# Optimization experiments

Hardware: AMD Instinct MI355X
Metric: run time of the kernel (lower is better)

The kernel has to match this reference:

```python
import jax, jax.numpy as jnp
import numpy as np

B = 8192
INPUT_DIM = 1024
HIDDEN = 4096
LATENT = 256
K = 16384  # codebook size
COMMIT = 0.25


def setup_inputs() -> dict:
    key = jax.random.key(0)
    ks = jax.random.split(key, 12)

    def lin(k, fan_in, fan_out):
        bound = 1.0 / np.sqrt(fan_in)
        kw, kb = jax.random.split(k)
        W = jax.random.uniform(kw, (fan_in, fan_out), jnp.float32, -bound, bound)
        b = jax.random.uniform(kb, (fan_out,), jnp.float32, -bound, bound)
        return W, b

    eW1, eb1 = lin(ks[0], INPUT_DIM, HIDDEN)
    eW2, eb2 = lin(ks[1], HIDDEN, HIDDEN)
    eW3, eb3 = lin(ks[2], HIDDEN, LATENT)
    dW1, db1 = lin(ks[3], LATENT, HIDDEN)
    dW2, db2 = lin(ks[4], HIDDEN, HIDDEN)
    dW3, db3 = lin(ks[5], HIDDEN, INPUT_DIM)
    codebook = jax.random.uniform(ks[6], (K, LATENT), jnp.float32, -1.0 / K, 1.0 / K)
    x = jax.random.normal(ks[7], (B, INPUT_DIM), jnp.float32)
    return {
        "x": x,
        "eW1": eW1, "eb1": eb1, "eW2": eW2, "eb2": eb2, "eW3": eW3, "eb3": eb3,
        "codebook": codebook,
        "dW1": dW1, "db1": db1, "dW2": dW2, "db2": db2, "dW3": dW3, "db3": db3,
    }


def _encoder(x, eW1, eb1, eW2, eb2, eW3, eb3):
    h = jax.nn.relu(x @ eW1 + eb1)          # dropout is identity in eval
    h = jax.nn.relu(h @ eW2 + eb2)
    return jnp.tanh(h @ eW3 + eb3)          # [B, LATENT]


def _decoder(z, dW1, db1, dW2, db2, dW3, db3):
    h = jax.nn.relu(z @ dW1 + db1)
    h = jax.nn.relu(h @ dW2 + db2)
    return h @ dW3 + db3                    # [B, INPUT_DIM]


def _vq(z, codebook):
    # pairwise squared distances: ||z||^2 + ||e||^2 - 2 z.e^T   -> [B, K]
    d = (jnp.sum(z * z, axis=1, keepdims=True)
         + jnp.sum(codebook * codebook, axis=1)
         - 2.0 * (z @ codebook.T))
    idx = jnp.argmin(d, axis=1)                              # [B]
    enc = jax.nn.one_hot(idx, K, dtype=jnp.float32)          # [B, K]
    q = enc @ codebook                                       # [B, LATENT]
    e_loss = jnp.mean((jax.lax.stop_gradient(q) - z) ** 2)
    q_loss = jnp.mean((q - jax.lax.stop_gradient(z)) ** 2)
    vq_loss = q_loss + COMMIT * e_loss
    q_st = z + jax.lax.stop_gradient(q - z)                  # straight-through
    avg_probs = jnp.mean(enc, axis=0)
    perplexity = jnp.exp(-jnp.sum(avg_probs * jnp.log(avg_probs + 1e-10)))
    return q_st, idx, vq_loss, perplexity


def reference(x, eW1, eb1, eW2, eb2, eW3, eb3, codebook,
              dW1, db1, dW2, db2, dW3, db3):
    z = _encoder(x, eW1, eb1, eW2, eb2, eW3, eb3)
    q, tokens, vq_loss, perplexity = _vq(z, codebook)
    recon = _decoder(q, dW1, db1, dW2, db2, dW3, db3)
    recon_loss = jnp.mean((recon - x) ** 2)
    total = vq_loss + recon_loss
    return recon, tokens, vq_loss, recon_loss, total, perplexity
```

## Files before the change

kernel.cpp:

```cpp
#include <hip/hip_runtime.h>
#include <stdint.h>

#define B_N 8192
#define D_IN 1024
#define D_HID 4096
#define D_LAT 256
#define K_CB 16384
#define VQ_NB (K_CB / 128)

typedef __attribute__((ext_vector_type(8))) short bf16x8;
typedef __attribute__((ext_vector_type(4))) float f32x4;

__device__ __forceinline__ unsigned short f2b(float v) {
  unsigned u = __float_as_uint(v);
  u += 0x7fffu + ((u >> 16) & 1u);
  return (unsigned short)(u >> 16);
}

#define XCD_SWIZZLE(bx, by)                                   \
  {                                                           \
    const int gx_ = gridDim.x, n_ = gx_ * gridDim.y;          \
    const int wg_ = (by)*gx_ + (bx);                          \
    const int q_ = n_ >> 3;                                   \
    const int s_ = (wg_ & 7) * q_ + (wg_ >> 3);               \
    (bx) = s_ % gx_;                                          \
    (by) = s_ / gx_;                                          \
  }

__device__ __forceinline__ void enc_big_body(
    const float* __restrict__ A, const float* __restrict__ Bm,
    const float* __restrict__ bias, float* __restrict__ C, int M, int N,
    int K) {
  __shared__ float As[16 * 260];
  __shared__ float Bs[16 * 128];
  const int tid = threadIdx.x;
  const int w = tid >> 6;
  const int tx = tid & 15, ty = tid >> 4;
  int bx = blockIdx.x, by = blockIdx.y;
  XCD_SWIZZLE(bx, by)
  const int m0 = by << 8, n0 = bx << 7;

  float acc[16][8];
#pragma unroll
  for (int i = 0; i < 16; ++i)
#pragma unroll
    for (int j = 0; j < 8; ++j) acc[i][j] = 0.0f;

  for (int k0 = 0; k0 < K; k0 += 16) {
#pragma unroll
    for (int r = 0; r < 4; ++r) {
      const int f = tid + (r << 8);
      const int m = f >> 2, kq = (f & 3) << 2;
      const float4 v = *(const float4*)(A + (size_t)(m0 + m) * K + k0 + kq);
      As[(kq + 0) * 260 + m] = v.x;
      As[(kq + 1) * 260 + m] = v.y;
      As[(kq + 2) * 260 + m] = v.z;
      As[(kq + 3) * 260 + m] = v.w;
    }
#pragma unroll
    for (int r = 0; r < 2; ++r) {
      const int f = tid + (r << 8);
      const float* gp = Bm + (size_t)(k0 + (f >> 5)) * N + n0 + ((f & 31) << 2);
      __builtin_amdgcn_global_load_lds((const unsigned int*)gp,
                                       (unsigned int*)&Bs[(r << 10) + (w << 8)],
                                       16, 0, 0);
    }
    __syncthreads();
#pragma unroll
    for (int kk = 0; kk < 16; ++kk) {
      float a[16], b[8];
#pragma unroll
      for (int q = 0; q < 4; ++q)
        *(float4*)(a + (q << 2)) =
            *(const float4*)(&As[kk * 260 + (q << 6) + (ty << 2)]);
      *(float4*)(b) = *(const float4*)(&Bs[kk * 128 + (tx << 2)]);
      *(float4*)(b + 4) = *(const float4*)(&Bs[kk * 128 + 64 + (tx << 2)]);
#pragma unroll
      for (int i = 0; i < 16; ++i)
#pragma unroll
        for (int j = 0; j < 8; ++j) acc[i][j] = fmaf(a[i], b[j], acc[i][j]);
    }
    __syncthreads();
  }

  float bb[8];
  *(float4*)(bb) = *(const float4*)(bias + n0 + (tx << 2));
  *(float4*)(bb + 4) = *(const float4*)(bias + n0 + 64 + (tx << 2));
#pragma unroll
  for (int i = 0; i < 16; ++i) {
    const int row = m0 + ((i >> 2) << 6) + (ty << 2) + (i & 3);
    float vrow[8];
#pragma unroll
    for (int j = 0; j < 8; ++j) vrow[j] = fmaxf(acc[i][j] + bb[j], 0.0f);
    *(float4*)(C + (size_t)row * N + n0 + (tx << 2)) = *(float4*)(vrow);
    *(float4*)(C + (size_t)row * N + n0 + 64 + (tx << 2)) = *(float4*)(vrow + 4);
  }
}

__global__ __launch_bounds__(256, 2) void enc1_k(const float* A, const float* B,
                                                 const float* bias, float* C,
                                                 int M, int N, int K) {
  enc_big_body(A, B, bias, C, M, N, K);
}
__global__ __launch_bounds__(256, 2) void enc2_k(const float* A, const float* B,
                                                 const float* bias, float* C,
                                                 int M, int N, int K) {
  enc_big_body(A, B, bias, C, M, N, K);
}

__global__ __launch_bounds__(256, 2) void enc_small_k(
    const float* __restrict__ A, const float* __restrict__ Bm,
    const float* __restrict__ bias, float* __restrict__ C, int M, int N,
    int K) {
  __shared__ float As[16][128];
  __shared__ float Bs[16][128];
  const int tid = threadIdx.x;
  const int tx = tid & 15, ty = tid >> 4;
  const int m0 = blockIdx.y << 7, n0 = blockIdx.x << 7;
  float acc[8][8];
#pragma unroll
  for (int i = 0; i < 8; ++i)
#pragma unroll
    for (int j = 0; j < 8; ++j) acc[i][j] = 0.0f;
  for (int k0 = 0; k0 < K; k0 += 16) {
#pragma unroll
    for (int r = 0; r < 2; ++r) {
      const int f = tid + (r << 8);
      const int m = f >> 2, kq = (f & 3) << 2;
      const float4 v = *(const float4*)(A + (size_t)(m0 + m) * K + k0 + kq);
      As[kq + 0][m] = v.x; As[kq + 1][m] = v.y;
      As[kq + 2][m] = v.z; As[kq + 3][m] = v.w;
    }
#pragma unroll
    for (int r = 0; r < 2; ++r) {
      const int f = tid + (r << 8);
      const int k = f >> 5, nq = (f & 31) << 2;
      *(float4*)(&Bs[k][nq]) =
          *(const float4*)(Bm + (size_t)(k0 + k) * N + n0 + nq);
    }
    __syncthreads();
#pragma unroll
    for (int kk = 0; kk < 16; ++kk) {
      float a[8], b[8];
      *(float4*)(a) = *(const float4*)(&As[kk][ty << 2]);
      *(float4*)(a + 4) = *(const float4*)(&As[kk][64 + (ty << 2)]);
      *(float4*)(b) = *(const float4*)(&Bs[kk][tx << 2]);
      *(float4*)(b + 4) = *(const float4*)(&Bs[kk][64 + (tx << 2)]);
#pragma unroll
      for (int i = 0; i < 8; ++i)
#pragma unroll
        for (int j = 0; j < 8; ++j) acc[i][j] = fmaf(a[i], b[j], acc[i][j]);
    }
    __syncthreads();
  }
  float bb[8];
  *(float4*)(bb) = *(const float4*)(bias + n0 + (tx << 2));
  *(float4*)(bb + 4) = *(const float4*)(bias + n0 + 64 + (tx << 2));
#pragma unroll
  for (int i = 0; i < 8; ++i) {
    const int row = m0 + ((i < 4) ? (ty << 2) + i : 64 + (ty << 2) + i - 4);
    float vrow[8];
#pragma unroll
    for (int j = 0; j < 8; ++j) vrow[j] = fmaxf(acc[i][j] + bb[j], 0.0f);
    *(float4*)(C + (size_t)row * N + n0 + (tx << 2)) = *(float4*)(vrow);
    *(float4*)(C + (size_t)row * N + n0 + 64 + (tx << 2)) = *(float4*)(vrow + 4);
  }
}

__global__ __launch_bounds__(256, 2) void enc3_part_k(
    const float* __restrict__ A, const float* __restrict__ B,
    float* __restrict__ P, int M, int K) {
  __shared__ float As[16][128];
  __shared__ float Bs[16][128];
  const int tid = threadIdx.x;
  const int tx = tid & 15, ty = tid >> 4;
  const int m0 = blockIdx.y << 7, n0 = blockIdx.x << 7;
  const int s = blockIdx.z;
  const int kbeg = s * (K >> 3), kend = kbeg + (K >> 3);
  float acc[8][8];
#pragma unroll
  for (int i = 0; i < 8; ++i)
#pragma unroll
    for (int j = 0; j < 8; ++j) acc[i][j] = 0.0f;
  for (int k0 = kbeg; k0 < kend; k0 += 16) {
#pragma unroll
    for (int r = 0; r < 2; ++r) {
      const int f = tid + (r << 8);
      const int m = f >> 2, kq = (f & 3) << 2;
      const float4 v = *(const float4*)(A + (size_t)(m0 + m) * K + k0 + kq);
      As[kq + 0][m] = v.x; As[kq + 1][m] = v.y;
      As[kq + 2][m] = v.z; As[kq + 3][m] = v.w;
    }
#pragma unroll
    for (int r = 0; r < 2; ++r) {
      const int f = tid + (r << 8);
      const int k = f >> 5, nq = (f & 31) << 2;
      *(float4*)(&Bs[k][nq]) =
          *(const float4*)(B + (size_t)(k0 + k) * D_LAT + n0 + nq);
    }
    __syncthreads();
#pragma unroll
    for (int kk = 0; kk < 16; ++kk) {
      float a[8], b[8];
      *(float4*)(a) = *(const float4*)(&As[kk][ty << 2]);
      *(float4*)(a + 4) = *(const float4*)(&As[kk][64 + (ty << 2)]);
      *(float4*)(b) = *(const float4*)(&Bs[kk][tx << 2]);
      *(float4*)(b + 4) = *(const float4*)(&Bs[kk][64 + (tx << 2)]);
#pragma unroll
      for (int i = 0; i < 8; ++i)
#pragma unroll
        for (int j = 0; j < 8; ++j) acc[i][j] = fmaf(a[i], b[j], acc[i][j]);
    }
    __syncthreads();
  }
  float* Ps = P + (size_t)s * M * D_LAT;
#pragma unroll
  for (int i = 0; i < 8; ++i) {
    const int row = m0 + ((i < 4) ? (ty << 2) + i : 64 + (ty << 2) + i - 4);
    *(float4*)(Ps + (size_t)row * D_LAT + n0 + (tx << 2)) = *(float4*)(&acc[i][0]);
    *(float4*)(Ps + (size_t)row * D_LAT + n0 + 64 + (tx << 2)) = *(float4*)(&acc[i][4]);
  }
}

__global__ void enc3_comb_k(const float* __restrict__ P,
                            const float* __restrict__ bias,
                            float* __restrict__ z, int M) {
  const size_t i4 = (size_t)blockIdx.x * blockDim.x + threadIdx.x;
  const size_t tot = (size_t)M * (D_LAT / 4);
  if (i4 >= tot) return;
  const size_t sstr = (size_t)M * (D_LAT / 4);
  const float4* Pv = (const float4*)P;
  float sx = 0.f, sy = 0.f, sz = 0.f, sw = 0.f;
#pragma unroll
  for (int s = 0; s < 8; ++s) {
    const float4 v = Pv[i4 + (size_t)s * sstr];
    sx += v.x; sy += v.y; sz += v.z; sw += v.w;
  }
  const int col = (int)((i4 << 2) & (D_LAT - 1));
  const float4 bb = *(const float4*)(bias + col);
  float4 o;
  o.x = tanhf(sx + bb.x);
  o.y = tanhf(sy + bb.y);
  o.z = tanhf(sz + bb.z);
  o.w = tanhf(sw + bb.w);
  ((float4*)z)[i4] = o;
}

__global__ __launch_bounds__(256, 2) void vq_k256(
    const float* __restrict__ A, const float* __restrict__ Bm,
    const float* __restrict__ zz, const float* __restrict__ ee,
    unsigned long long* __restrict__ keys2) {
  __shared__ float As[16 * 260];
  __shared__ float Bs[16 * 132];
  const int tid = threadIdx.x;
  const int tx = tid & 15, ty = tid >> 4;
  int bx = blockIdx.x, by = blockIdx.y;
  XCD_SWIZZLE(bx, by)
  const int m0 = by << 8, n0 = bx << 7;
  const int K = D_LAT;

  float acc[16][8];
#pragma unroll
  for (int i = 0; i < 16; ++i)
#pragma unroll
    for (int j = 0; j < 8; ++j) acc[i][j] = 0.0f;

  for (int k0 = 0; k0 < K; k0 += 16) {
#pragma unroll
    for (int r = 0; r < 4; ++r) {
      const int f = tid + (r << 8);
      const int m = f >> 2, kq = (f & 3) << 2;
      const float4 v = *(const float4*)(A + (size_t)(m0 + m) * K + k0 + kq);
      As[(kq + 0) * 260 + m] = v.x;
      As[(kq + 1) * 260 + m] = v.y;
      As[(kq + 2) * 260 + m] = v.z;
      As[(kq + 3) * 260 + m] = v.w;
    }
#pragma unroll
    for (int r = 0; r < 2; ++r) {
      const int f = tid + (r << 8);
      const int n = f >> 2, kq = (f & 3) << 2;
      const float4 v = *(const float4*)(Bm + (size_t)(n0 + n) * K + k0 + kq);
      Bs[(kq + 0) * 132 + n] = v.x;
      Bs[(kq + 1) * 132 + n] = v.y;
      Bs[(kq + 2) * 132 + n] = v.z;
      Bs[(kq + 3) * 132 + n] = v.w;
    }
    __syncthreads();
#pragma unroll
    for (int kk = 0; kk < 16; ++kk) {
      float a[16], b[8];
#pragma unroll
      for (int q = 0; q < 4; ++q)
        *(float4*)(a + (q << 2)) =
            *(const float4*)(&As[kk * 260 + (q << 6) + (ty << 2)]);
      *(float4*)(b) = *(const float4*)(&Bs[kk * 132 + (tx << 2)]);
      *(float4*)(b + 4) = *(const float4*)(&Bs[kk * 132 + 64 + (tx << 2)]);
#pragma unroll
      for (int i = 0; i < 16; ++i)
#pragma unroll
        for (int j = 0; j < 8; ++j) acc[i][j] = fmaf(a[i], b[j], acc[i][j]);
    }
    __syncthreads();
  }

  float zr[16];
#pragma unroll
  for (int i = 0; i < 16; ++i)
    zr[i] = zz[m0 + ((i >> 2) << 6) + (ty << 2) + (i & 3)];
  float ev[8];
  *(float4*)(ev) = *(const float4*)(ee + n0 + (tx << 2));
  *(float4*)(ev + 4) = *(const float4*)(ee + n0 + 64 + (tx << 2));
#pragma unroll
  for (int i = 0; i < 16; ++i) {
    unsigned long long bk = ~0ull;
#pragma unroll
    for (int j = 0; j < 8; ++j) {
      const int col = n0 + ((j >> 2) << 6) + (tx << 2) + (j & 3);
      const float t = zr[i] + ev[j];
      const float d = t - 2.0f * acc[i][j];
      unsigned u = __float_as_uint(d);
      u = (u & 0x80000000u) ? ~u : (u | 0x80000000u);
      const unsigned long long key = ((unsigned long long)u << 32) | (unsigned)col;
      bk = key < bk ? key : bk;
    }
#pragma unroll
    for (int s = 1; s <= 8; s <<= 1) {
      const unsigned long long o = __shfl_xor(bk, s);
      if (o < bk) bk = o;
    }
    if (tx == 0) {
      const int row = m0 + ((i >> 2) << 6) + (ty << 2) + (i & 3);
      keys2[(size_t)row * VQ_NB + bx] = bk;
    }
  }
}

__global__ void vq_red_k(const unsigned long long* __restrict__ keys2,
                         unsigned long long* __restrict__ keys) {
  const int row = (int)((blockIdx.x * blockDim.x + threadIdx.x) >> 6);
  const int lane = threadIdx.x & 63;
  if (row >= B_N) return;
  unsigned long long a = keys2[(size_t)row * VQ_NB + lane];
  const unsigned long long b = keys2[(size_t)row * VQ_NB + 64 + lane];
  a = b < a ? b : a;
#pragma unroll
  for (int s = 32; s; s >>= 1) {
    const unsigned long long o = __shfl_xor(a, s);
    a = o < a ? o : a;
  }
  if (lane == 0) keys[row] = a;
}

template <int EPI>
__device__ __forceinline__ void mgemm_body(
    const unsigned short* __restrict__ A, const unsigned short* __restrict__ Bt,
    const float* __restrict__ bias, void* __restrict__ Cout, int M, int N,
    int K, const float* __restrict__ xref, double* __restrict__ accums) {
  __shared__ __align__(16) unsigned short As[4096];
  __shared__ __align__(16) unsigned short Bs[4096];
  const int tid = threadIdx.x;
  const int w = tid >> 6, l = tid & 63;
  const int wr = w >> 1, wc = w & 1;
  const int g = l >> 4, tx = l & 15;
  int bx = blockIdx.x, by = blockIdx.y;
  XCD_SWIZZLE(bx, by)
  const int m0 = by << 7, n0 = bx << 7;

  f32x4 acc[4][4];
#pragma unroll
  for (int i = 0; i < 4; ++i)
#pragma unroll
    for (int j = 0; j < 4; ++j) acc[i][j] = (f32x4)0.0f;

  for (int k0 = 0; k0 < K; k0 += 32) {
#pragma unroll
    for (int c = 0; c < 2; ++c) {
      const int f = tid + (c << 8);
      const unsigned short* ga =
          A + (size_t)(m0 + (f >> 2)) * K + k0 + ((f & 3) << 3);
      __builtin_amdgcn_global_load_lds((const unsigned int*)ga,
                                       (unsigned int*)&As[(c << 11) + (w << 9)],
                                       16, 0, 0);
      const unsigned short* gb =
          Bt + (size_t)(n0 + (f >> 2)) * K + k0 + ((f & 3) << 3);
      __builtin_amdgcn_global_load_lds((const unsigned int*)gb,
                                       (unsigned int*)&Bs[(c << 11) + (w << 9)],
                                       16, 0, 0);
    }
    __syncthreads();
    bf16x8 af[4], bfv[4];
#pragma unroll
    for (int f = 0; f < 4; ++f) {
      af[f] = *(const bf16x8*)&As[((wr << 6) + (f << 4) + tx) * 32 + (g << 3)];
      bfv[f] = *(const bf16x8*)&Bs[((wc << 6) + (f << 4) + tx) * 32 + (g << 3)];
    }
#pragma unroll
    for (int fm = 0; fm < 4; ++fm)
#pragma unroll
      for (int fn = 0; fn < 4; ++fn)
        acc[fm][fn] = __builtin_amdgcn_mfma_f32_16x16x32_bf16(
            af[fm], bfv[fn], acc[fm][fn], 0, 0, 0);
    __syncthreads();
  }

  double lsum = 0.0;
#pragma unroll
  for (int fm = 0; fm < 4; ++fm) {
    const int row0 = m0 + (wr << 6) + (fm << 4) + (g << 2);
#pragma unroll
    for (int fn = 0; fn < 4; ++fn) {
      const int col = n0 + (wc << 6) + (fn << 4) + tx;
      const float bb = bias[col];
#pragma unroll
      for (int r = 0; r < 4; ++r) {
        float v = acc[fm][fn][r] + bb;
        if (EPI == 0) {
          v = fmaxf(v, 0.0f);
          ((unsigned short*)Cout)[(size_t)(row0 + r) * N + col] = f2b(v);
        } else {
          const float xr = xref[(size_t)(row0 + r) * N + col];
          const float df = v - xr;
          lsum += (double)df * (double)df;
          ((float*)Cout)[(size_t)(row0 + r) * N + col] = v;
        }
      }
    }
  }
  if (EPI == 1) {
#pragma unroll
    for (int o = 32; o; o >>= 1) lsum += __shfl_down(lsum, o);
    if (l == 0) atomicAdd(accums + 1, lsum);
  }
}

__global__ __launch_bounds__(256, 2) void dec1_k(const unsigned short* A,
                                                 const unsigned short* Bt,
                                                 const float* bias,
                                                 unsigned short* C, int M,
                                                 int N, int K) {
  mgemm_body<0>(A, Bt, bias, C, M, N, K, nullptr, nullptr);
}
__global__ __launch_bounds__(256, 2) void dec2_k(const unsigned short* A,
                                                 const unsigned short* Bt,
                                                 const float* bias,
                                                 unsigned short* C, int M,
                                                 int N, int K) {
  mgemm_body<0>(A, Bt, bias, C, M, N, K, nullptr, nullptr);
}
__global__ __launch_bounds__(256, 2) void dec3_k(const unsigned short* A,
                                                 const unsigned short* Bt,
                                                 const float* bias, float* C,
                                                 int M, int N, int K,
                                                 const float* xref,
                                                 double* accums) {
  mgemm_body<1>(A, Bt, bias, C, M, N, K, xref, accums);
}

__global__ void castT_k(const float* __restrict__ W,
                        unsigned short* __restrict__ out, int K, int N) {
  __shared__ float t[32][33];
  const int tx = threadIdx.x & 31, ty4 = threadIdx.x >> 5;
  const int nb = blockIdx.x << 5, kb = blockIdx.y << 5;
#pragma unroll
  for (int r = 0; r < 4; ++r) {
    const int k = (ty4 << 2) + r;
    t[k][tx] = W[(size_t)(kb + k) * N + nb + tx];
  }
  __syncthreads();
#pragma unroll
  for (int r = 0; r < 4; ++r) {
    const int n = (ty4 << 2) + r;
    out[(size_t)(nb + n) * K + kb + tx] = f2b(t[tx][n]);
  }
}

__global__ void rowsumsq(const float* __restrict__ v, float* __restrict__ out,
                         int rows) {
  const int w = (int)((blockIdx.x * blockDim.x + threadIdx.x) >> 6);
  const int lane = threadIdx.x & 63;
  if (w >= rows) return;
  const float4 x = *(const float4*)(v + (size_t)w * 256 + (lane << 2));
  float s = ((x.x * x.x + x.y * x.y) + x.z * x.z) + x.w * x.w;
#pragma unroll
  for (int o = 32; o; o >>= 1) s += __shfl_down(s, o);
  if (lane == 0) out[w] = s;
}

__global__ void finalize_vq(const unsigned long long* __restrict__ keys,
                            const float* __restrict__ z,
                            const float* __restrict__ cb,
                            unsigned short* __restrict__ qst_bf,
                            float* __restrict__ tok, int* __restrict__ counts,
                            double* __restrict__ accums) {
  const int row = (int)((blockIdx.x * blockDim.x + threadIdx.x) >> 6);
  const int lane = threadIdx.x & 63;
  if (row >= B_N) return;
  const int idx = (int)(keys[row] & 0xffffffffull);
  const float4 zv = *(const float4*)(z + (size_t)row * 256 + (lane << 2));
  const float4 evv = *(const float4*)(cb + (size_t)idx * 256 + (lane << 2));
  float4 q;
  double s = 0.0;
  float d;
  d = evv.x - zv.x; q.x = zv.x + d; s += (double)d * (double)d;
  d = evv.y - zv.y; q.y = zv.y + d; s += (double)d * (double)d;
  d = evv.z - zv.z; q.z = zv.z + d; s += (double)d * (double)d;
  d = evv.w - zv.w; q.w = zv.w + d; s += (double)d * (double)d;
  ushort4 qb;
  qb.x = f2b(q.x); qb.y = f2b(q.y); qb.z = f2b(q.z); qb.w = f2b(q.w);
  *(ushort4*)(qst_bf + (size_t)row * 256 + (lane << 2)) = qb;
#pragma unroll
  for (int o = 32; o; o >>= 1) s += __shfl_down(s, o);
  if (lane == 0) {
    atomicAdd(accums + 0, s);
    tok[row] = (float)idx;
    atomicAdd(counts + idx, 1);
  }
}

__global__ void finalize_scalars(const int* __restrict__ counts,
                                 const double* __restrict__ accums,
                                 float* __restrict__ outs) {
  __shared__ double red[256];
  double h = 0.0;
  for (int k = threadIdx.x; k < K_CB; k += 256) {
    const float p = (float)counts[k] * (1.0f / 8192.0f);
    const float t = p * logf(p + 1e-10f);
    h += (double)t;
  }
  red[threadIdx.x] = h;
  __syncthreads();
  for (int s = 128; s; s >>= 1) {
    if ((int)threadIdx.x < s) red[threadIdx.x] += red[threadIdx.x + s];
    __syncthreads();
  }
  if (threadIdx.x == 0) {
    const float perp = expf((float)(-red[0]));
    const float m1 = (float)(accums[0] * (1.0 / ((double)B_N * (double)D_LAT)));
    const float vq = m1 + 0.25f * m1;
    const float rl = (float)(accums[1] * (1.0 / ((double)B_N * (double)D_IN)));
    outs[0] = vq;
    outs[1] = rl;
    outs[2] = vq + rl;
    outs[3] = perp;
  }
}

extern "C" void kernel_launch(void* const* d_in, const int* in_sizes, int n_in,
                              void* d_out, int out_size, void* d_ws,
                              size_t ws_size, hipStream_t stream) {
  (void)in_sizes; (void)n_in; (void)out_size;
  const float* x   = (const float*)d_in[0];
  const float* eW1 = (const float*)d_in[1];
  const float* eb1 = (const float*)d_in[2];
  const float* eW2 = (const float*)d_in[3];
  const float* eb2 = (const float*)d_in[4];
  const float* eW3 = (const float*)d_in[5];
  const float* eb3 = (const float*)d_in[6];
  const float* cb  = (const float*)d_in[7];
  const float* dW1 = (const float*)d_in[8];
  const float* db1 = (const float*)d_in[9];
  const float* dW2 = (const float*)d_in[10];
  const float* db2 = (const float*)d_in[11];
  const float* dW3 = (const float*)d_in[12];
  const float* db3 = (const float*)d_in[13];
  float* out = (float*)d_out;

  char* ws = (char*)d_ws;
  const size_t OFF_Z      = 0;
  const size_t OFF_EEV    = OFF_Z + (size_t)B_N * D_LAT * 4;
  const size_t OFF_ZZV    = OFF_EEV + (size_t)K_CB * 4;
  const size_t OFF_KEYS   = OFF_ZZV + (size_t)B_N * 4;
  const size_t OFF_COUNTS = OFF_KEYS + (size_t)B_N * 8;
  const size_t OFF_ACC    = OFF_COUNTS + (size_t)K_CB * 4;
  const size_t OFF_QB     = OFF_ACC + 256;
  const size_t OFF_K2     = OFF_QB + (size_t)B_N * D_LAT * 2;
  const size_t OFF_H      = OFF_K2 + (size_t)B_N * VQ_NB * 8;

  float* z    = (float*)(ws + OFF_Z);
  float* eev  = (float*)(ws + OFF_EEV);
  float* zzv  = (float*)(ws + OFF_ZZV);
  unsigned long long* keys = (unsigned long long*)(ws + OFF_KEYS);
  int* counts = (int*)(ws + OFF_COUNTS);
  double* accums = (double*)(ws + OFF_ACC);
  unsigned short* qst_bf = (unsigned short*)(ws + OFF_QB);
  unsigned long long* keys2 = (unsigned long long*)(ws + OFF_K2);

  int c_enc = 256;
  for (int c = 8192; c >= 256; c >>= 1)
    if (OFF_H + 2ull * c * D_HID * 4 <= ws_size) { c_enc = c; break; }
  float* hA = (float*)(ws + OFF_H);
  float* hB = hA + (size_t)c_enc * D_HID;
  float* P3 = hA;

  const size_t SZ_WB1 = (size_t)D_HID * D_LAT * 2;
  const size_t SZ_WB2 = (size_t)D_HID * D_HID * 2;
  const size_t SZ_WB3 = (size_t)D_IN * D_HID * 2;
  const size_t OFF_DECH = OFF_H + SZ_WB1 + SZ_WB2 + SZ_WB3;
  int c_dec = 128;
  for (int c = 8192; c >= 128; c >>= 1)
    if (OFF_DECH + 2ull * c * D_HID * 2 <= ws_size) { c_dec = c; break; }
  unsigned short* wB1 = (unsigned short*)(ws + OFF_H);
  unsigned short* wB2 = (unsigned short*)(ws + OFF_H + SZ_WB1);
  unsigned short* wB3 = (unsigned short*)(ws + OFF_H + SZ_WB1 + SZ_WB2);
  unsigned short* hbfA = (unsigned short*)(ws + OFF_DECH);
  unsigned short* hbfB = hbfA + (size_t)c_dec * D_HID;

  float* tok_out = out + (size_t)B_N * D_IN;
  float* scal_out = tok_out + B_N;

  hipMemsetAsync(counts, 0, (size_t)K_CB * 4, stream);
  hipMemsetAsync(accums, 0, 2 * sizeof(double), stream);

  rowsumsq<<<(K_CB * 64) / 256, 256, 0, stream>>>(cb, eev, K_CB);

  const bool big = (c_enc >= 4096);
  for (int c0 = 0; c0 < B_N; c0 += c_enc) {
    if (big) {
      enc1_k<<<dim3(D_HID / 128, c_enc / 256), 256, 0, stream>>>(
          x + (size_t)c0 * D_IN, eW1, eb1, hA, c_enc, D_HID, D_IN);
      enc2_k<<<dim3(D_HID / 128, c_enc / 256), 256, 0, stream>>>(
          hA, eW2, eb2, hB, c_enc, D_HID, D_HID);
    } else {
      const dim3 gH(D_HID / 128, c_enc / 128);
      enc_small_k<<<gH, 256, 0, stream>>>(x + (size_t)c0 * D_IN, eW1, eb1, hA,
                                          c_enc, D_HID, D_IN);
      enc_small_k<<<gH, 256, 0, stream>>>(hA, eW2, eb2, hB, c_enc, D_HID,
                                          D_HID);
    }
    enc3_part_k<<<dim3(D_LAT / 128, c_enc / 128, 8), 256, 0, stream>>>(
        hB, eW3, P3, c_enc, D_HID);
    enc3_comb_k<<<(c_enc * (D_LAT / 4) + 255) / 256, 256, 0, stream>>>(
        P3, eb3, z + (size_t)c0 * D_LAT, c_enc);
  }

  rowsumsq<<<(B_N * 64) / 256, 256, 0, stream>>>(z, zzv, B_N);

  vq_k256<<<dim3(VQ_NB, B_N / 256), 256, 0, stream>>>(z, cb, zzv, eev, keys2);
  vq_red_k<<<(B_N * 64) / 256, 256, 0, stream>>>(keys2, keys);
  finalize_vq<<<(B_N * 64) / 256, 256, 0, stream>>>(keys, z, cb, qst_bf,
                                                    tok_out, counts, accums);

  castT_k<<<dim3(D_HID / 32, D_LAT / 32), 256, 0, stream>>>(dW1, wB1, D_LAT, D_HID);
  castT_k<<<dim3(D_HID / 32, D_HID / 32), 256, 0, stream>>>(dW2, wB2, D_HID, D_HID);
  castT_k<<<dim3(D_IN / 32, D_HID / 32), 256, 0, stream>>>(dW3, wB3, D_HID, D_IN);

  for (int c0 = 0; c0 < B_N; c0 += c_dec) {
    const dim3 gH(D_HID / 128, c_dec / 128);
    dec1_k<<<gH, 256, 0, stream>>>(qst_bf + (size_t)c0 * D_LAT, wB1, db1, hbfA,
                                   c_dec, D_HID, D_LAT);
    dec2_k<<<gH, 256, 0, stream>>>(hbfA, wB2, db2, hbfB, c_dec, D_HID, D_HID);
    dec3_k<<<dim3(D_IN / 128, c_dec / 128), 256, 0, stream>>>(
        hbfB, wB3, db3, out + (size_t)c0 * D_IN, c_dec, D_IN, D_HID,
        x + (size_t)c0 * D_IN, accums);
  }

  finalize_scalars<<<1, 256, 0, stream>>>(counts, accums, scal_out);
}
```

Measured before the change: 5.649 ms.

## Keep encoder activations transposed and load A tiles via global_load_lds

```diff
diff --git a/kernel.cpp b/kernel.cpp
--- a/kernel.cpp
+++ b/kernel.cpp
@@ -27,11 +27,29 @@
     (by) = s_ / gx_;                                          \
   }
 
-__device__ __forceinline__ void enc_big_body(
-    const float* __restrict__ A, const float* __restrict__ Bm,
-    const float* __restrict__ bias, float* __restrict__ C, int M, int N,
+__global__ void transF_k(const float* __restrict__ in, float* __restrict__ out,
+                         int R, int C) {
+  __shared__ float t[32][33];
+  const int tx = threadIdx.x & 31, ty4 = threadIdx.x >> 5;
+  const int rb = blockIdx.y << 5, cb_ = blockIdx.x << 5;
+#pragma unroll
+  for (int r = 0; r < 4; ++r) {
+    const int lr = (ty4 << 2) + r;
+    t[lr][tx] = in[(size_t)(rb + lr) * C + cb_ + tx];
+  }
+  __syncthreads();
+#pragma unroll
+  for (int r = 0; r < 4; ++r) {
+    const int lr = (ty4 << 2) + r;
+    out[(size_t)(cb_ + lr) * R + rb + tx] = t[tx][lr];
+  }
+}
+
+__device__ __forceinline__ void enc_bigT_body(
+    const float* __restrict__ AT_, const float* __restrict__ Bm,
+    const float* __restrict__ bias, float* __restrict__ CT, int M, int N,
     int K) {
-  __shared__ float As[16 * 260];
+  __shared__ float As[16 * 256];
   __shared__ float Bs[16 * 128];
   const int tid = threadIdx.x;
   const int w = tid >> 6;
@@ -50,12 +68,10 @@
 #pragma unroll
     for (int r = 0; r < 4; ++r) {
       const int f = tid + (r << 8);
-      const int m = f >> 2, kq = (f & 3) << 2;
-      const float4 v = *(const float4*)(A + (size_t)(m0 + m) * K + k0 + kq);
-      As[(kq + 0) * 260 + m] = v.x;
-      As[(kq + 1) * 260 + m] = v.y;
-      As[(kq + 2) * 260 + m] = v.z;
-      As[(kq + 3) * 260 + m] = v.w;
+      const float* gp = AT_ + (size_t)(k0 + (f >> 6)) * M + m0 + ((f & 63) << 2);
+      __builtin_amdgcn_global_load_lds((const unsigned int*)gp,
+                                       (unsigned int*)&As[(r << 10) + (w << 8)],
+                                       16, 0, 0);
     }
 #pragma unroll
     for (int r = 0; r < 2; ++r) {
@@ -72,7 +88,7 @@
 #pragma unroll
       for (int q = 0; q < 4; ++q)
         *(float4*)(a + (q << 2)) =
-            *(const float4*)(&As[kk * 260 + (q << 6) + (ty << 2)]);
+            *(const float4*)(&As[kk * 256 + (q << 6) + (ty << 2)]);
       *(float4*)(b) = *(const float4*)(&Bs[kk * 128 + (tx << 2)]);
       *(float4*)(b + 4) = *(const float4*)(&Bs[kk * 128 + 64 + (tx << 2)]);
 #pragma unroll
@@ -87,25 +103,31 @@
   *(float4*)(bb) = *(const float4*)(bias + n0 + (tx << 2));
   *(float4*)(bb + 4) = *(const float4*)(bias + n0 + 64 + (tx << 2));
 #pragma unroll
-  for (int i = 0; i < 16; ++i) {
-    const int row = m0 + ((i >> 2) << 6) + (ty << 2) + (i & 3);
-    float vrow[8];
-#pragma unroll
-    for (int j = 0; j < 8; ++j) vrow[j] = fmaxf(acc[i][j] + bb[j], 0.0f);
-    *(float4*)(C + (size_t)row * N + n0 + (tx << 2)) = *(float4*)(vrow);
-    *(float4*)(C + (size_t)row * N + n0 + 64 + (tx << 2)) = *(float4*)(vrow + 4);
-  }
-}
-
-__global__ __launch_bounds__(256, 2) void enc1_k(const float* A, const float* B,
-                                                 const float* bias, float* C,
+  for (int j = 0; j < 8; ++j) {
+    const int col = n0 + ((j >> 2) << 6) + (tx << 2) + (j & 3);
+#pragma unroll
+    for (int q = 0; q < 4; ++q) {
+      float vq4[4];
+#pragma unroll
+      for (int r = 0; r < 4; ++r)
+        vq4[r] = fmaxf(acc[(q << 2) + r][j] + bb[j], 0.0f);
+      *(float4*)(CT + (size_t)col * M + m0 + (q << 6) + (ty << 2)) =
+          *(float4*)(vq4);
+    }
+  }
+}
+
+__global__ __launch_bounds__(256, 2) void enc1_k(const float* AT_,
+                                                 const float* B,
+                                                 const float* bias, float* CT,
                                                  int M, int N, int K) {
-  enc_big_body(A, B, bias, C, M, N, K);
-}
-__global__ __launch_bounds__(256, 2) void enc2_k(const float* A, const float* B,
-                                                 const float* bias, float* C,
+  enc_bigT_body(AT_, B, bias, CT, M, N, K);
+}
+__global__ __launch_bounds__(256, 2) void enc2_k(const float* AT_,
+                                                 const float* B,
+                                                 const float* bias, float* CT,
                                                  int M, int N, int K) {
-  enc_big_body(A, B, bias, C, M, N, K);
+  enc_bigT_body(AT_, B, bias, CT, M, N, K);
 }
 
 __global__ __launch_bounds__(256, 2) void enc_small_k(
@@ -167,12 +189,14 @@
   }
 }
 
+template <bool AT>
 __global__ __launch_bounds__(256, 2) void enc3_part_k(
     const float* __restrict__ A, const float* __restrict__ B,
-    float* __restrict__ P, int M, int K) {
-  __shared__ float As[16][128];
-  __shared__ float Bs[16][128];
+    float* __restrict__ P, int M, int K, int Mstr) {
+  __shared__ float As[16 * 128];
+  __shared__ float Bs[16 * 128];
   const int tid = threadIdx.x;
+  const int w = tid >> 6;
   const int tx = tid & 15, ty = tid >> 4;
   const int m0 = blockIdx.y << 7, n0 = blockIdx.x << 7;
   const int s = blockIdx.z;
@@ -183,29 +207,42 @@
 #pragma unroll
     for (int j = 0; j < 8; ++j) acc[i][j] = 0.0f;
   for (int k0 = kbeg; k0 < kend; k0 += 16) {
+    if (AT) {
+#pragma unroll
+      for (int r = 0; r < 2; ++r) {
+        const int f = tid + (r << 8);
+        const float* gp =
+            A + (size_t)(k0 + (f >> 5)) * Mstr + m0 + ((f & 31) << 2);
+        __builtin_amdgcn_global_load_lds(
+            (const unsigned int*)gp, (unsigned int*)&As[(r << 10) + (w << 8)],
+            16, 0, 0);
+      }
+    } else {
+#pragma unroll
+      for (int r = 0; r < 2; ++r) {
+        const int f = tid + (r << 8);
+        const int m = f >> 2, kq = (f & 3) << 2;
+        const float4 v = *(const float4*)(A + (size_t)(m0 + m) * K + k0 + kq);
+        As[(kq + 0) * 128 + m] = v.x; As[(kq + 1) * 128 + m] = v.y;
+        As[(kq + 2) * 128 + m] = v.z; As[(kq + 3) * 128 + m] = v.w;
+      }
+    }
 #pragma unroll
     for (int r = 0; r < 2; ++r) {
       const int f = tid + (r << 8);
-      const int m = f >> 2, kq = (f & 3) << 2;
-      const float4 v = *(const float4*)(A + (size_t)(m0 + m) * K + k0 + kq);
-      As[kq + 0][m] = v.x; As[kq + 1][m] = v.y;
-      As[kq + 2][m] = v.z; As[kq + 3][m] = v.w;
-    }
-#pragma unroll
-    for (int r = 0; r < 2; ++r) {
-      const int f = tid + (r << 8);
-      const int k = f >> 5, nq = (f & 31) << 2;
-      *(float4*)(&Bs[k][nq]) =
-          *(const float4*)(B + (size_t)(k0 + k) * D_LAT + n0 + nq);
+      const float* gp = B + (size_t)(k0 + (f >> 5)) * D_LAT + n0 + ((f & 31) << 2);
+      __builtin_amdgcn_global_load_lds((const unsigned int*)gp,
+                                       (unsigned int*)&Bs[(r << 10) + (w << 8)],
+                                       16, 0, 0);
     }
     __syncthreads();
 #pragma unroll
     for (int kk = 0; kk < 16; ++kk) {
       float a[8], b[8];
-      *(float4*)(a) = *(const float4*)(&As[kk][ty << 2]);
-      *(float4*)(a + 4) = *(const float4*)(&As[kk][64 + (ty << 2)]);
-      *(float4*)(b) = *(const float4*)(&Bs[kk][tx << 2]);
-      *(float4*)(b + 4) = *(const float4*)(&Bs[kk][64 + (tx << 2)]);
+      *(float4*)(a) = *(const float4*)(&As[kk * 128 + (ty << 2)]);
+      *(float4*)(a + 4) = *(const float4*)(&As[kk * 128 + 64 + (ty << 2)]);
+      *(float4*)(b) = *(const float4*)(&Bs[kk * 128 + (tx << 2)]);
+      *(float4*)(b + 4) = *(const float4*)(&Bs[kk * 128 + 64 + (tx << 2)]);
 #pragma unroll
       for (int i = 0; i < 8; ++i)
 #pragma unroll
@@ -247,17 +284,17 @@
 }
 
 __global__ __launch_bounds__(256, 2) void vq_k256(
-    const float* __restrict__ A, const float* __restrict__ Bm,
+    const float* __restrict__ zT, const float* __restrict__ cbT,
     const float* __restrict__ zz, const float* __restrict__ ee,
     unsigned long long* __restrict__ keys2) {
-  __shared__ float As[16 * 260];
-  __shared__ float Bs[16 * 132];
+  __shared__ float As[16 * 256];
+  __shared__ float Bs[16 * 128];
   const int tid = threadIdx.x;
+  const int w = tid >> 6;
   const int tx = tid & 15, ty = tid >> 4;
   int bx = blockIdx.x, by = blockIdx.y;
   XCD_SWIZZLE(bx, by)
   const int m0 = by << 8, n0 = bx << 7;
-  const int K = D_LAT;
 
   float acc[16][8];
 #pragma unroll
@@ -265,26 +302,22 @@
 #pragma unroll
     for (int j = 0; j < 8; ++j) acc[i][j] = 0.0f;
 
-  for (int k0 = 0; k0 < K; k0 += 16) {
+  for (int k0 = 0; k0 < D_LAT; k0 += 16) {
 #pragma unroll
     for (int r = 0; r < 4; ++r) {
       const int f = tid + (r << 8);
-      const int m = f >> 2, kq = (f & 3) << 2;
-      const float4 v = *(const float4*)(A + (size_t)(m0 + m) * K + k0 + kq);
-      As[(kq + 0) * 260 + m] = v.x;
-      As[(kq + 1) * 260 + m] = v.y;
-      As[(kq + 2) * 260 + m] = v.z;
-      As[(kq + 3) * 260 + m] = v.w;
+      const float* gp = zT + (size_t)(k0 + (f >> 6)) * B_N + m0 + ((f & 63) << 2);
+      __builtin_amdgcn_global_load_lds((const unsigned int*)gp,
+                                       (unsigned int*)&As[(r << 10) + (w << 8)],
+                                       16, 0, 0);
     }
 #pragma unroll
     for (int r = 0; r < 2; ++r) {
       const int f = tid + (r << 8);
-      const int n = f >> 2, kq = (f & 3) << 2;
-      const float4 v = *(const float4*)(Bm + (size_t)(n0 + n) * K + k0 + kq);
-      Bs[(kq + 0) * 132 + n] = v.x;
-      Bs[(kq + 1) * 132 + n] = v.y;
-      Bs[(kq + 2) * 132 + n] = v.z;
-      Bs[(kq + 3) * 132 + n] = v.w;
+      const float* gp = cbT + (size_t)(k0 + (f >> 5)) * K_CB + n0 + ((f & 31) << 2);
+      __builtin_amdgcn_global_load_lds((const unsigned int*)gp,
+                                       (unsigned int*)&Bs[(r << 10) + (w << 8)],
+                                       16, 0, 0);
     }
     __syncthreads();
 #pragma unroll
@@ -293,9 +326,9 @@
 #pragma unroll
       for (int q = 0; q < 4; ++q)
         *(float4*)(a + (q << 2)) =
-            *(const float4*)(&As[kk * 260 + (q << 6) + (ty << 2)]);
-      *(float4*)(b) = *(const float4*)(&Bs[kk * 132 + (tx << 2)]);
-      *(float4*)(b + 4) = *(const float4*)(&Bs[kk * 132 + 64 + (tx << 2)]);
+            *(const float4*)(&As[kk * 256 + (q << 6) + (ty << 2)]);
+      *(float4*)(b) = *(const float4*)(&Bs[kk * 128 + (tx << 2)]);
+      *(float4*)(b + 4) = *(const float4*)(&Bs[kk * 128 + 64 + (tx << 2)]);
 #pragma unroll
       for (int i = 0; i < 16; ++i)
 #pragma unroll
@@ -591,7 +624,10 @@
     if (OFF_H + 2ull * c * D_HID * 4 <= ws_size) { c_enc = c; break; }
   float* hA = (float*)(ws + OFF_H);
   float* hB = hA + (size_t)c_enc * D_HID;
-  float* P3 = hA;
+  float* xT  = hB;
+  float* P3  = hA;
+  float* zT  = hA;
+  float* cbT = hB;
 
   const size_t SZ_WB1 = (size_t)D_HID * D_LAT * 2;
   const size_t SZ_WB2 = (size_t)D_HID * D_HID * 2;
@@ -614,29 +650,37 @@
 
   rowsumsq<<<(K_CB * 64) / 256, 256, 0, stream>>>(cb, eev, K_CB);
 
-  const bool big = (c_enc >= 4096);
-  for (int c0 = 0; c0 < B_N; c0 += c_enc) {
-    if (big) {
-      enc1_k<<<dim3(D_HID / 128, c_enc / 256), 256, 0, stream>>>(
-          x + (size_t)c0 * D_IN, eW1, eb1, hA, c_enc, D_HID, D_IN);
-      enc2_k<<<dim3(D_HID / 128, c_enc / 256), 256, 0, stream>>>(
-          hA, eW2, eb2, hB, c_enc, D_HID, D_HID);
-    } else {
+  const bool big = (c_enc >= 8192);
+  if (big) {
+    transF_k<<<dim3(D_IN / 32, B_N / 32), 256, 0, stream>>>(x, xT, B_N, D_IN);
+    enc1_k<<<dim3(D_HID / 128, B_N / 256), 256, 0, stream>>>(
+        xT, eW1, eb1, hA , B_N, D_HID, D_IN);
+    enc2_k<<<dim3(D_HID / 128, B_N / 256), 256, 0, stream>>>(
+        hA, eW2, eb2, hB , B_N, D_HID, D_HID);
+    enc3_part_k<true><<<dim3(D_LAT / 128, B_N / 128, 8), 256, 0, stream>>>(
+        hB, eW3, P3, B_N, D_HID, B_N);
+    enc3_comb_k<<<(B_N * (D_LAT / 4) + 255) / 256, 256, 0, stream>>>(
+        P3, eb3, z, B_N);
+  } else {
+    for (int c0 = 0; c0 < B_N; c0 += c_enc) {
       const dim3 gH(D_HID / 128, c_enc / 128);
       enc_small_k<<<gH, 256, 0, stream>>>(x + (size_t)c0 * D_IN, eW1, eb1, hA,
                                           c_enc, D_HID, D_IN);
       enc_small_k<<<gH, 256, 0, stream>>>(hA, eW2, eb2, hB, c_enc, D_HID,
                                           D_HID);
-    }
-    enc3_part_k<<<dim3(D_LAT / 128, c_enc / 128, 8), 256, 0, stream>>>(
-        hB, eW3, P3, c_enc, D_HID);
-    enc3_comb_k<<<(c_enc * (D_LAT / 4) + 255) / 256, 256, 0, stream>>>(
-        P3, eb3, z + (size_t)c0 * D_LAT, c_enc);
-  }
-
+      enc3_part_k<false><<<dim3(D_LAT / 128, c_enc / 128, 8), 256, 0, stream>>>(
+          hB, eW3, P3, c_enc, D_HID, 0);
+      enc3_comb_k<<<(c_enc * (D_LAT / 4) + 255) / 256, 256, 0, stream>>>(
+          P3, eb3, z + (size_t)c0 * D_LAT, c_enc);
+    }
+  }
+
+  transF_k<<<dim3(D_LAT / 32, B_N / 32), 256, 0, stream>>>(z, zT, B_N, D_LAT);
+  transF_k<<<dim3(D_LAT / 32, K_CB / 32), 256, 0, stream>>>(cb, cbT, K_CB,
+                                                            D_LAT);
   rowsumsq<<<(B_N * 64) / 256, 256, 0, stream>>>(z, zzv, B_N);
 
-  vq_k256<<<dim3(VQ_NB, B_N / 256), 256, 0, stream>>>(z, cb, zzv, eev, keys2);
+  vq_k256<<<dim3(VQ_NB, B_N / 256), 256, 0, stream>>>(zT, cbT, zzv, eev, keys2);
   vq_red_k<<<(B_N * 64) / 256, 256, 0, stream>>>(keys2, keys);
   finalize_vq<<<(B_N * 64) / 256, 256, 0, stream>>>(keys, z, cb, qst_bf,
                                                     tok_out, counts, accums);
```

New measurement: 5.456 ms. 1.04x faster.
